# Kernel tuning notes

Hardware: AMD Instinct MI355X
Metric: run time of the kernel (lower is better)

Reference implementation:

```python
import jax, jax.numpy as jnp
import numpy as np

N_CLOSEST = 16
OBJECTNESS_THRESH = 0.75


def _masked_softmax(att, mask):
    # softmax over axis 1 restricted to mask; rows with empty mask -> all zeros
    neg = jnp.where(mask, att, -jnp.inf)
    m = jnp.max(neg, axis=1, keepdims=True)
    m = jnp.where(jnp.isfinite(m), m, 0.0)
    e = jnp.where(mask, jnp.exp(att - m), 0.0)
    d = jnp.sum(e, axis=1, keepdims=True)
    return jnp.where(d > 0, e / jnp.maximum(d, 1e-30), 0.0)


def _forward(aggregated_vote_features, ref_obj_features, objectness_scores,
             ref_center_label, aggregated_vote_xyz, emb_table, init_emb,
             W_enc_att, b_enc_att, W_dec_att, b_dec_att, w_full_att, b_full_att,
             W_ih, b_ih, W_hh, b_hh, W_init_h, b_init_h, W_init_c, b_init_c,
             W_fbeta, b_fbeta, W_fc, b_fc, lang_indices, lang_len):
    B, K, VD = aggregated_vote_features.shape
    T = lang_indices.shape[1]

    # --- objectness + distance (top-k closest) masking ---
    objness = jax.nn.softmax(objectness_scores, axis=-1)[:, :, -1]      # [B,K]
    omask = objness > OBJECTNESS_THRESH
    dist = jnp.linalg.norm(ref_center_label[:, None, :] - aggregated_vote_xyz, axis=2)
    dist = jnp.where(omask, dist, jnp.inf)
    closest = -jax.lax.top_k(-dist, N_CLOSEST)[0]                        # k smallest
    max_d = jnp.max(closest, axis=1, keepdims=True)
    object_mask = omask & (dist <= max_d)                                # [B,K]

    enc = aggregated_vote_features                                       # [B,K,VD]
    init_in = jnp.concatenate([enc.mean(axis=1), ref_obj_features], axis=1)
    h0 = init_in @ W_init_h.T + b_init_h                                 # [B,D]
    c0 = init_in @ W_init_c.T + b_init_c

    # encoder attention projection is constant over timesteps
    att1 = jnp.einsum('bkv,av->bka', enc, W_enc_att) + b_enc_att         # [B,K,A]

    # teacher-forcing inputs: <unk> init embedding then caption embeddings
    E = init_emb.shape[-1]
    emb = jnp.concatenate(
        [jnp.broadcast_to(init_emb, (B, E))[:, None, :], emb_table[lang_indices]],
        axis=1)                                                          # [B,T+1,E]
    emb_steps = jnp.swapaxes(emb[:, :T], 0, 1)                           # [T,B,E]
    t_steps = jnp.arange(T)

    def step(carry, xs):
        h, c = carry
        emb_t, t = xs
        # attention
        att2 = h @ W_dec_att.T + b_dec_att                               # [B,A]
        att = jax.nn.relu(att1 + att2[:, None, :]) @ w_full_att + b_full_att[0]  # [B,K]
        alpha = _masked_softmax(att, object_mask)
        awe = jnp.einsum('bkv,bk->bv', enc, alpha)                       # [B,VD]
        gate = jax.nn.sigmoid(h @ W_fbeta.T + b_fbeta)
        awe = gate * awe
        # LSTMCell (torch gate order i,f,g,o)
        x = jnp.concatenate([emb_t, awe, ref_obj_features], axis=1)      # [B,E+VD+OD]
        gates = x @ W_ih.T + b_ih + h @ W_hh.T + b_hh
        i, f, g, o = jnp.split(gates, 4, axis=1)
        c_new = jax.nn.sigmoid(f) * c + jax.nn.sigmoid(i) * jnp.tanh(g)
        h_new = jax.nn.sigmoid(o) * jnp.tanh(c_new)
        # only samples with length > t are decoded (masked equivalent of batch_size_t)
        active = (t < lang_len)[:, None]
        preds = jnp.where(active, h_new @ W_fc.T + b_fc, 0.0)            # [B,V]
        alpha_o = jnp.where(active, alpha, 0.0)
        h = jnp.where(active, h_new, h)
        c = jnp.where(active, c_new, c)
        return (h, c), (preds, alpha_o)

    _, (preds_seq, alpha_seq) = jax.lax.scan(step, (h0, c0), (emb_steps, t_steps))
    predictions = jnp.transpose(preds_seq, (1, 2, 0))                    # [B,V,T]
    alphas = jnp.transpose(alpha_seq, (1, 0, 2))                         # [B,T,K]
    return predictions, alphas, object_mask


def setup_inputs() -> dict:
    key = jax.random.key(0)
    ks = jax.random.split(key, 20)
    B, K, VD, OD, E, A, D, V, T = 128, 128, 128, 256, 300, 512, 512, 4000, 32
    ENC = VD + OD

    def rn(k, shape, s=1.0):
        return jax.random.normal(k, shape, jnp.float32) * s

    return {
        'aggregated_vote_features': rn(ks[0], (B, K, VD)),
        'ref_obj_features': rn(ks[1], (B, OD)),
        'objectness_scores': rn(ks[2], (B, K, 2)),
        'ref_center_label': rn(ks[3], (B, 3)),
        'aggregated_vote_xyz': rn(ks[4], (B, K, 3)),
        'lang_indices': jax.random.randint(ks[5], (B, T), 0, V),
        'lang_len': jax.random.randint(ks[6], (B,), 1, T + 1),
        'emb_table': rn(ks[7], (V, E), 0.1),
        'init_emb': rn(ks[8], (1, E), 0.1),
        'W_enc_att': rn(ks[9], (A, VD), 0.05), 'b_enc_att': jnp.zeros((A,)),
        'W_dec_att': rn(ks[10], (A, D), 0.05), 'b_dec_att': jnp.zeros((A,)),
        'w_full_att': rn(ks[11], (A,), 0.05), 'b_full_att': jnp.zeros((1,)),
        'W_ih': rn(ks[12], (4 * D, E + ENC), 0.05), 'b_ih': jnp.zeros((4 * D,)),
        'W_hh': rn(ks[13], (4 * D, D), 0.05), 'b_hh': jnp.zeros((4 * D,)),
        'W_init_h': rn(ks[14], (D, ENC), 0.05), 'b_init_h': jnp.zeros((D,)),
        'W_init_c': rn(ks[15], (D, ENC), 0.05), 'b_init_c': jnp.zeros((D,)),
        'W_fbeta': rn(ks[16], (VD, D), 0.05), 'b_fbeta': jnp.zeros((VD,)),
        'W_fc': rn(ks[17], (V, D), 0.1), 'b_fc': jnp.zeros((V,)),
    }


def reference(aggregated_vote_features, ref_obj_features, objectness_scores,
              ref_center_label, aggregated_vote_xyz, lang_indices, lang_len,
              emb_table, init_emb, W_enc_att, b_enc_att, W_dec_att, b_dec_att,
              w_full_att, b_full_att, W_ih, b_ih, W_hh, b_hh, W_init_h, b_init_h,
              W_init_c, b_init_c, W_fbeta, b_fbeta, W_fc, b_fc):
    return _forward(aggregated_vote_features, ref_obj_features, objectness_scores,
                    ref_center_label, aggregated_vote_xyz, emb_table, init_emb,
                    W_enc_att, b_enc_att, W_dec_att, b_dec_att, w_full_att, b_full_att,
                    W_ih, b_ih, W_hh, b_hh, W_init_h, b_init_h, W_init_c, b_init_c,
                    W_fbeta, b_fbeta, W_fc, b_fc, lang_indices, lang_len)
```

## Files before the change

kernel.cpp:

```cpp
#include <hip/hip_runtime.h>
#include <hip/hip_bf16.h>
#include <math.h>

#define XKTOT 1196
#define XKP   1216

static __device__ __forceinline__ float sigmoidf_(float x){ return 1.f/(1.f+expf(-x)); }

__global__ __launch_bounds__(256) void k_transpose(const float* __restrict__ in,
                                                   float* __restrict__ out, int R, int C) {
  __shared__ float tile[32][33];
  int c0 = blockIdx.x * 32, r0 = blockIdx.y * 32;
  int tx = threadIdx.x & 31, ty = threadIdx.x >> 5;
  for (int i = 0; i < 32; i += 8) {
    int r = r0 + ty + i, c = c0 + tx;
    tile[ty + i][tx] = (r < R && c < C) ? in[(size_t)r * C + c] : 0.f;
  }
  __syncthreads();
  for (int i = 0; i < 32; i += 8) {
    int c = c0 + ty + i, r = r0 + tx;
    if (c < C && r < R) out[(size_t)c * R + r] = tile[tx][ty + i];
  }
}

__global__ __launch_bounds__(256) void k_wcat(const float* __restrict__ W_ih,
                                              const float* __restrict__ W_hh,
                                              float* __restrict__ Wcat) {
  int j = blockIdx.x;
  for (int c = threadIdx.x; c < XKP; c += 256) {
    float v;
    if (c < 684)        v = W_ih[(size_t)j * 684 + c];
    else if (c < 1196)  v = W_hh[(size_t)j * 512 + (c - 684)];
    else                v = 0.f;
    Wcat[(size_t)j * XKP + c] = v;
  }
}

__global__ __launch_bounds__(128) void k_mask(const float* __restrict__ objs,
                                              const float* __restrict__ rcl,
                                              const float* __restrict__ avx,
                                              const float* __restrict__ enc,
                                              float* __restrict__ maskf,
                                              float* __restrict__ encmean,
                                              float* __restrict__ out_mask) {
  int b = blockIdx.x, k = threadIdx.x;
  __shared__ float dsh[128];
  __shared__ float maxd;
  float s0 = objs[(size_t)(b * 128 + k) * 2 + 0];
  float s1 = objs[(size_t)(b * 128 + k) * 2 + 1];
  float mx = fmaxf(s0, s1);
  float e0 = expf(s0 - mx), e1 = expf(s1 - mx);
  float p  = e1 / (e0 + e1);
  bool om  = p > 0.75f;
  float dx = rcl[b * 3 + 0] - avx[(size_t)(b * 128 + k) * 3 + 0];
  float dy = rcl[b * 3 + 1] - avx[(size_t)(b * 128 + k) * 3 + 1];
  float dz = rcl[b * 3 + 2] - avx[(size_t)(b * 128 + k) * 3 + 2];
  float dist = sqrtf(dx * dx + dy * dy + dz * dz);
  float dm = om ? dist : INFINITY;
  dsh[k] = dm;
  __syncthreads();
  float v = dm; int clt = 0, cle = 0;
  for (int j = 0; j < 128; j++) { float o = dsh[j]; clt += (o < v); cle += (o <= v); }
  if (clt < 16 && cle >= 16) maxd = v;
  __syncthreads();
  bool msk = om && (dm <= maxd);
  maskf[b * 128 + k]    = msk ? 1.f : 0.f;
  out_mask[b * 128 + k] = msk ? 1.f : 0.f;
  float s = 0.f;
  for (int kk = 0; kk < 128; kk++) s += enc[(size_t)(b * 128 + kk) * 128 + k];
  encmean[b * 128 + k] = s * (1.f / 128.f);
}

__global__ __launch_bounds__(512) void k_init(const float* __restrict__ encm,
                                              const float* __restrict__ rof,
                                              const float* __restrict__ wihT,
                                              const float* __restrict__ wicT,
                                              const float* __restrict__ bh,
                                              const float* __restrict__ bc,
                                              float* __restrict__ h, float* __restrict__ c) {
  int b = blockIdx.x, d = threadIdx.x;
  __shared__ float xin[384];
  if (d < 128) xin[d] = encm[b * 128 + d];
  else if (d < 384) xin[d] = rof[(size_t)b * 256 + (d - 128)];
  __syncthreads();
  float ah = bh[d], ac = bc[d];
  for (int i = 0; i < 384; i++) {
    float x = xin[i];
    ah += x * wihT[(size_t)i * 512 + d];
    ac += x * wicT[(size_t)i * 512 + d];
  }
  h[(size_t)b * 512 + d] = ah;
  c[(size_t)b * 512 + d] = ac;
}

__global__ __launch_bounds__(512) void k_att1(const float* __restrict__ enc,
                                              const float* __restrict__ weT,
                                              const float* __restrict__ b_enc,
                                              float* __restrict__ att1) {
  int b = blockIdx.x >> 3, k0 = (blockIdx.x & 7) * 16;
  int a = threadIdx.x;
  __shared__ float es[16][128];
  for (int i = threadIdx.x; i < 16 * 128; i += 512)
    es[i >> 7][i & 127] = enc[(size_t)(b * 128 + k0 + (i >> 7)) * 128 + (i & 127)];
  __syncthreads();
  float acc[16];
  float bb = b_enc[a];
#pragma unroll
  for (int kk = 0; kk < 16; kk++) acc[kk] = bb;
  for (int i = 0; i < 128; i++) {
    float w = weT[(size_t)i * 512 + a];
#pragma unroll
    for (int kk = 0; kk < 16; kk++) acc[kk] += w * es[kk][i];
  }
#pragma unroll
  for (int kk = 0; kk < 16; kk++)
    att1[(size_t)(b * 128 + k0 + kk) * 512 + a] = acc[kk];
}

__global__ __launch_bounds__(512) void k_step_att(
    const float* __restrict__ att1, const float* __restrict__ h,
    const float* __restrict__ wdT, const float* __restrict__ b_dec,
    const float* __restrict__ wfull, const float* __restrict__ bfull,
    const float* __restrict__ enc, const float* __restrict__ maskf,
    const float* __restrict__ wfbT, const float* __restrict__ b_fbeta,
    const float* __restrict__ rof, const float* __restrict__ embt,
    const float* __restrict__ iemb, const int* __restrict__ lidx,
    const int* __restrict__ llen, float* __restrict__ X,
    float* __restrict__ alphas_out, int t) {
  int b = blockIdx.x, tid = threadIdx.x;
  __shared__ float hs[512], att2[512], wf[512], attk[128], alph[128], awes[128];
  __shared__ float red1[2], red2[2];
  hs[tid] = h[(size_t)b * 512 + tid];
  wf[tid] = wfull[tid];
  __syncthreads();
  {
    float acc = b_dec[tid];
    for (int i = 0; i < 512; i++) acc += hs[i] * wdT[(size_t)i * 512 + tid];
    att2[tid] = acc;
  }
  __syncthreads();
  int k = tid >> 2, j = tid & 3;
  {
    const float4* a1 = (const float4*)(att1 + (size_t)(b * 128 + k) * 512 + j * 128);
    float s = 0.f;
#pragma unroll 4
    for (int i = 0; i < 32; i++) {
      float4 v = a1[i];
      int base = j * 128 + i * 4;
      s += fmaxf(v.x + att2[base + 0], 0.f) * wf[base + 0];
      s += fmaxf(v.y + att2[base + 1], 0.f) * wf[base + 1];
      s += fmaxf(v.z + att2[base + 2], 0.f) * wf[base + 2];
      s += fmaxf(v.w + att2[base + 3], 0.f) * wf[base + 3];
    }
    s += __shfl_xor(s, 1);
    s += __shfl_xor(s, 2);
    if (j == 0) attk[k] = s + bfull[0];
  }
  __syncthreads();
  float mk = 0.f, av = 0.f;
  if (tid < 128) { mk = maskf[b * 128 + tid]; av = attk[tid]; }
  float nv = (tid < 128 && mk != 0.f) ? av : -INFINITY;
  float wm = nv;
#pragma unroll
  for (int o = 32; o > 0; o >>= 1) wm = fmaxf(wm, __shfl_xor(wm, o));
  if (tid < 128 && (tid & 63) == 0) red1[tid >> 6] = wm;
  __syncthreads();
  float m = fmaxf(red1[0], red1[1]);
  float e = 0.f;
  if (tid < 128 && mk != 0.f) e = expf(av - m);
  float sred = e;
#pragma unroll
  for (int o = 32; o > 0; o >>= 1) sred += __shfl_xor(sred, o);
  if (tid < 128 && (tid & 63) == 0) red2[tid >> 6] = sred;
  __syncthreads();
  float dsum = red2[0] + red2[1];
  float alpha = (dsum > 0.f) ? e / fmaxf(dsum, 1e-30f) : 0.f;
  int active = t < llen[b];
  if (tid < 128) {
    alph[tid] = alpha;
    alphas_out[(size_t)(b * 32 + t) * 128 + tid] = active ? alpha : 0.f;
  }
  __syncthreads();
  float awe_v = 0.f;
  if (tid < 128) {
    for (int kk = 0; kk < 128; kk++)
      awe_v += alph[kk] * enc[(size_t)(b * 128 + kk) * 128 + tid];
  }
  {
    int v = tid >> 2;
    float g = 0.f;
    for (int ii = 0; ii < 128; ii++) {
      int i = j * 128 + ii;
      g += hs[i] * wfbT[(size_t)i * 128 + v];
    }
    g += __shfl_xor(g, 1);
    g += __shfl_xor(g, 2);
    if (j == 0) attk[v] = sigmoidf_(g + b_fbeta[v]);
  }
  __syncthreads();
  if (tid < 128) awes[tid] = awe_v * attk[tid];
  __syncthreads();
  const float* esrc = (t == 0) ? iemb : (embt + (size_t)lidx[b * 32 + (t - 1)] * 300);
  for (int c = tid; c < XKP; c += 512) {
    float val;
    if (c < 300)       val = esrc[c];
    else if (c < 428)  val = awes[c - 300];
    else if (c < 684)  val = rof[(size_t)b * 256 + (c - 428)];
    else if (c < 1196) val = hs[c - 684];
    else               val = 0.f;
    X[(size_t)b * XKP + c] = val;
  }
}

__global__ __launch_bounds__(256) void k_gemm(const float* __restrict__ Am, int lda,
                                              const float* __restrict__ Bw, int ldb, int N,
                                              int klen, float* __restrict__ Cpart, int ldc) {
  int n0 = blockIdx.x * 64;
  int m0 = blockIdx.y * 64;
  int kstart = blockIdx.z * klen;
  float* Cout = Cpart + (size_t)blockIdx.z * 128 * ldc;
  int tc = threadIdx.x & 15, tr = threadIdx.x >> 4;
  __shared__ float As[16][68];
  __shared__ float Bs[16][68];
  float acc[4][4];
#pragma unroll
  for (int r = 0; r < 4; r++)
#pragma unroll
    for (int cc = 0; cc < 4; cc++) acc[r][cc] = 0.f;
  int srow = threadIdx.x >> 2, sq = threadIdx.x & 3;
  bool bok = (n0 + srow) < N;
  const float* aSrc = Am + (size_t)(m0 + srow) * lda + sq * 4;
  const float* bSrc = Bw + (size_t)(n0 + srow) * ldb + sq * 4;
  for (int k0 = kstart; k0 < kstart + klen; k0 += 16) {
    float4 va = *(const float4*)(aSrc + k0);
    float4 vb;
    if (bok) vb = *(const float4*)(bSrc + k0);
    else { vb.x = vb.y = vb.z = vb.w = 0.f; }
    As[sq * 4 + 0][srow] = va.x; As[sq * 4 + 1][srow] = va.y;
    As[sq * 4 + 2][srow] = va.z; As[sq * 4 + 3][srow] = va.w;
    Bs[sq * 4 + 0][srow] = vb.x; Bs[sq * 4 + 1][srow] = vb.y;
    Bs[sq * 4 + 2][srow] = vb.z; Bs[sq * 4 + 3][srow] = vb.w;
    __syncthreads();
#pragma unroll
    for (int ki = 0; ki < 16; ki++) {
      float4 a  = *(const float4*)&As[ki][tr * 4];
      float4 bv = *(const float4*)&Bs[ki][tc * 4];
      acc[0][0] += a.x * bv.x; acc[0][1] += a.x * bv.y; acc[0][2] += a.x * bv.z; acc[0][3] += a.x * bv.w;
      acc[1][0] += a.y * bv.x; acc[1][1] += a.y * bv.y; acc[1][2] += a.y * bv.z; acc[1][3] += a.y * bv.w;
      acc[2][0] += a.z * bv.x; acc[2][1] += a.z * bv.y; acc[2][2] += a.z * bv.z; acc[2][3] += a.z * bv.w;
      acc[3][0] += a.w * bv.x; acc[3][1] += a.w * bv.y; acc[3][2] += a.w * bv.z; acc[3][3] += a.w * bv.w;
    }
    __syncthreads();
  }
#pragma unroll
  for (int r = 0; r < 4; r++) {
    int mi = m0 + tr * 4 + r;
#pragma unroll
    for (int cc = 0; cc < 4; cc++) {
      int n = n0 + tc * 4 + cc;
      if (n < N) Cout[(size_t)mi * ldc + n] = acc[r][cc];
    }
  }
}

__global__ __launch_bounds__(256) void k_lstm(const float* __restrict__ gpart,
                                              const float* __restrict__ b_ih,
                                              const float* __restrict__ b_hh,
                                              const int* __restrict__ llen,
                                              float* __restrict__ h, float* __restrict__ c,
                                              int t) {
  int idx = blockIdx.x * 256 + threadIdx.x;
  int b = idx >> 9, d = idx & 511;
  if (t >= llen[b]) return;
  float g4[4];
#pragma unroll
  for (int g = 0; g < 4; g++) {
    int j = g * 512 + d;
    float s = b_ih[j] + b_hh[j];
#pragma unroll
    for (int z = 0; z < 4; z++) s += gpart[((size_t)z * 128 + b) * 2048 + j];
    g4[g] = s;
  }
  float i_ = sigmoidf_(g4[0]);
  float f_ = sigmoidf_(g4[1]);
  float gg = tanhf(g4[2]);
  float o_ = sigmoidf_(g4[3]);
  float cn = f_ * c[idx] + i_ * gg;
  float hn = o_ * tanhf(cn);
  c[idx] = cn;
  h[idx] = hn;
}

__global__ __launch_bounds__(256) void k_fc_red(const float* __restrict__ fpart,
                                                const float* __restrict__ b_fc,
                                                const int* __restrict__ llen,
                                                float* __restrict__ dst, int t, int direct) {
  int idx = blockIdx.x * 256 + threadIdx.x;
  int b = idx / 4000, v = idx - b * 4000;
  float s = 0.f;
  if (t < llen[b])
    s = fpart[(size_t)b * 4000 + v] + fpart[(size_t)(128 + b) * 4000 + v] + b_fc[v];
  if (direct) dst[((size_t)b * 4000 + v) * 32 + t] = s;
  else        dst[((size_t)t * 128 + b) * 4000 + v] = s;
}

__global__ __launch_bounds__(256) void k_out_tr(const float* __restrict__ predsT,
                                                float* __restrict__ out) {
  __shared__ float tile[32][33];
  int b = blockIdx.y, v0 = blockIdx.x * 32;
  int tx = threadIdx.x & 31, ty = threadIdx.x >> 5;
  for (int i = 0; i < 32; i += 8) {
    int tt = ty + i;
    tile[tt][tx] = predsT[((size_t)tt * 128 + b) * 4000 + v0 + tx];
  }
  __syncthreads();
  for (int i = 0; i < 32; i += 8) {
    int v = v0 + ty + i;
    out[((size_t)b * 4000 + v) * 32 + tx] = tile[tx][ty + i];
  }
}

extern "C" void kernel_launch(void* const* d_in, const int* in_sizes, int n_in,
                              void* d_out, int out_size, void* d_ws, size_t ws_size,
                              hipStream_t stream) {
  (void)in_sizes; (void)n_in; (void)out_size;
  const float* avf   = (const float*)d_in[0];
  const float* rof   = (const float*)d_in[1];
  const float* objs  = (const float*)d_in[2];
  const float* rcl   = (const float*)d_in[3];
  const float* avx   = (const float*)d_in[4];
  const int*   lidx  = (const int*)d_in[5];
  const int*   llen  = (const int*)d_in[6];
  const float* embt  = (const float*)d_in[7];
  const float* iemb  = (const float*)d_in[8];
  const float* W_enc = (const float*)d_in[9];
  const float* b_enc = (const float*)d_in[10];
  const float* W_dec = (const float*)d_in[11];
  const float* b_dec = (const float*)d_in[12];
  const float* wfull = (const float*)d_in[13];
  const float* bfull = (const float*)d_in[14];
  const float* W_ih  = (const float*)d_in[15];
  const float* b_ih  = (const float*)d_in[16];
  const float* W_hh  = (const float*)d_in[17];
  const float* b_hh  = (const float*)d_in[18];
  const float* W_inh = (const float*)d_in[19];
  const float* b_inh = (const float*)d_in[20];
  const float* W_inc = (const float*)d_in[21];
  const float* b_inc = (const float*)d_in[22];
  const float* W_fb  = (const float*)d_in[23];
  const float* b_fb  = (const float*)d_in[24];
  const float* W_fc  = (const float*)d_in[25];
  const float* b_fc  = (const float*)d_in[26];

  float* ws = (float*)d_ws;
  size_t f = 0;
  auto A8 = [&](size_t n) { size_t o = f; f += (n + 63) & ~(size_t)63; return o; };
  float* att1  = ws + A8((size_t)128 * 128 * 512);
  float* Wcat  = ws + A8((size_t)2048 * XKP);
  float* wdT   = ws + A8(512 * 512);
  float* weT   = ws + A8(128 * 512);
  float* wihT  = ws + A8(384 * 512);
  float* wicT  = ws + A8(384 * 512);
  float* wfbT  = ws + A8(512 * 128);
  float* hbuf  = ws + A8(128 * 512);
  float* cbuf  = ws + A8(128 * 512);
  float* Xbuf  = ws + A8((size_t)128 * XKP);
  float* maskf = ws + A8(128 * 128);
  float* encm  = ws + A8(128 * 128);
  float* gpart = ws + A8((size_t)4 * 128 * 2048);
  float* fpart = ws + A8((size_t)2 * 128 * 4000);
  float* predsT = ws + A8((size_t)32 * 128 * 4000);
  bool useT = ws_size >= f * sizeof(float);

  float* out_pred  = (float*)d_out;
  float* out_alpha = out_pred + (size_t)16384000;
  float* out_mask  = out_alpha + (size_t)524288;

  k_transpose<<<dim3(16, 16), 256, 0, stream>>>(W_dec, wdT, 512, 512);
  k_transpose<<<dim3(4, 16),  256, 0, stream>>>(W_enc, weT, 512, 128);
  k_transpose<<<dim3(12, 16), 256, 0, stream>>>(W_inh, wihT, 512, 384);
  k_transpose<<<dim3(12, 16), 256, 0, stream>>>(W_inc, wicT, 512, 384);
  k_transpose<<<dim3(16, 4),  256, 0, stream>>>(W_fb, wfbT, 128, 512);
  k_wcat<<<2048, 256, 0, stream>>>(W_ih, W_hh, Wcat);
  k_mask<<<128, 128, 0, stream>>>(objs, rcl, avx, avf, maskf, encm, out_mask);
  k_init<<<128, 512, 0, stream>>>(encm, rof, wihT, wicT, b_inh, b_inc, hbuf, cbuf);
  k_att1<<<1024, 512, 0, stream>>>(avf, weT, b_enc, att1);

  for (int t = 0; t < 32; t++) {
    k_step_att<<<128, 512, 0, stream>>>(att1, hbuf, wdT, b_dec, wfull, bfull,
        avf, maskf, wfbT, b_fb, rof, embt, iemb, lidx, llen, Xbuf, out_alpha, t);
    k_gemm<<<dim3(32, 2, 4), 256, 0, stream>>>(Xbuf, XKP, Wcat, XKP, 2048, 304, gpart, 2048);
    k_lstm<<<256, 256, 0, stream>>>(gpart, b_ih, b_hh, llen, hbuf, cbuf, t);
    k_gemm<<<dim3(63, 2, 2), 256, 0, stream>>>(hbuf, 512, W_fc, 512, 4000, 256, fpart, 4000);
    k_fc_red<<<2000, 256, 0, stream>>>(fpart, b_fc, llen,
                                       useT ? predsT : out_pred, t, useT ? 0 : 1);
  }
  if (useT) k_out_tr<<<dim3(125, 128), 256, 0, stream>>>(predsT, out_pred);
}
```

Baseline: 2.730 ms.

## Move LSTM gate, FC and attention projections onto bf16 MFMA with split precision

Replaces the fp32 SIMT GEMMs with bf16 MFMA kernels. The LSTM gate GEMM uses hi/lo split bf16 (three products) to keep near-fp32 accuracy and fuses the LSTM cell update into its epilogue. The FC projection is also fused with bias, masking and store, which removes the split-K partial buffers and the separate reduction kernels. The encoder attention projection and FC now run in plain bf16, which adds conversion kernels and some rounding error.

```diff
diff --git a/kernel.cpp b/kernel.cpp
--- a/kernel.cpp
+++ b/kernel.cpp
@@ -5,7 +5,13 @@
 #define XKTOT 1196
 #define XKP   1216
 
+typedef unsigned short u16;
+typedef short bf16x8 __attribute__((ext_vector_type(8)));
+typedef float f32x4 __attribute__((ext_vector_type(4)));
+
 static __device__ __forceinline__ float sigmoidf_(float x){ return 1.f/(1.f+expf(-x)); }
+static __device__ __forceinline__ u16 f2bf(float x){ __hip_bfloat16 h = __float2bfloat16(x); return *reinterpret_cast<u16*>(&h); }
+static __device__ __forceinline__ float bf2f(u16 u){ __hip_bfloat16 h; *reinterpret_cast<u16*>(&h) = u; return __bfloat162float(h); }
 
 __global__ __launch_bounds__(256) void k_transpose(const float* __restrict__ in,
                                                    float* __restrict__ out, int R, int C) {
@@ -23,16 +29,28 @@
   }
 }
 
-__global__ __launch_bounds__(256) void k_wcat(const float* __restrict__ W_ih,
-                                              const float* __restrict__ W_hh,
-                                              float* __restrict__ Wcat) {
-  int j = blockIdx.x;
+__global__ __launch_bounds__(256) void k_cvt(const float* __restrict__ in,
+                                             u16* __restrict__ out, int n) {
+  for (int i = blockIdx.x * 256 + threadIdx.x; i < n; i += gridDim.x * 256)
+    out[i] = f2bf(in[i]);
+}
+
+__global__ __launch_bounds__(256) void k_wcat_split(const float* __restrict__ W_ih,
+                                                    const float* __restrict__ W_hh,
+                                                    u16* __restrict__ Whi,
+                                                    u16* __restrict__ Wlo) {
+  int np = blockIdx.x;
+  int d = np >> 2, g = np & 3;
+  int j = g * 512 + d;
   for (int c = threadIdx.x; c < XKP; c += 256) {
     float v;
     if (c < 684)        v = W_ih[(size_t)j * 684 + c];
     else if (c < 1196)  v = W_hh[(size_t)j * 512 + (c - 684)];
     else                v = 0.f;
-    Wcat[(size_t)j * XKP + c] = v;
+    u16 hi = f2bf(v);
+    u16 lo = f2bf(v - bf2f(hi));
+    Whi[(size_t)np * XKP + c] = hi;
+    Wlo[(size_t)np * XKP + c] = lo;
   }
 }
 
@@ -77,7 +95,8 @@
                                               const float* __restrict__ wicT,
                                               const float* __restrict__ bh,
                                               const float* __restrict__ bc,
-                                              float* __restrict__ h, float* __restrict__ c) {
+                                              float* __restrict__ h, float* __restrict__ c,
+                                              u16* __restrict__ hb16) {
   int b = blockIdx.x, d = threadIdx.x;
   __shared__ float xin[384];
   if (d < 128) xin[d] = encm[b * 128 + d];
@@ -89,32 +108,45 @@
     ah += x * wihT[(size_t)i * 512 + d];
     ac += x * wicT[(size_t)i * 512 + d];
   }
-  h[(size_t)b * 512 + d] = ah;
-  c[(size_t)b * 512 + d] = ac;
-}
-
-__global__ __launch_bounds__(512) void k_att1(const float* __restrict__ enc,
-                                              const float* __restrict__ weT,
-                                              const float* __restrict__ b_enc,
-                                              float* __restrict__ att1) {
-  int b = blockIdx.x >> 3, k0 = (blockIdx.x & 7) * 16;
-  int a = threadIdx.x;
-  __shared__ float es[16][128];
-  for (int i = threadIdx.x; i < 16 * 128; i += 512)
-    es[i >> 7][i & 127] = enc[(size_t)(b * 128 + k0 + (i >> 7)) * 128 + (i & 127)];
-  __syncthreads();
-  float acc[16];
-  float bb = b_enc[a];
-#pragma unroll
-  for (int kk = 0; kk < 16; kk++) acc[kk] = bb;
-  for (int i = 0; i < 128; i++) {
-    float w = weT[(size_t)i * 512 + a];
-#pragma unroll
-    for (int kk = 0; kk < 16; kk++) acc[kk] += w * es[kk][i];
-  }
-#pragma unroll
-  for (int kk = 0; kk < 16; kk++)
-    att1[(size_t)(b * 128 + k0 + kk) * 512 + a] = acc[kk];
+  size_t idx = (size_t)b * 512 + d;
+  h[idx] = ah;
+  c[idx] = ac;
+  hb16[idx] = f2bf(ah);
+}
+
+__global__ __launch_bounds__(256) void k_att1m(const u16* __restrict__ enc16,
+                                               const u16* __restrict__ We16,
+                                               const float* __restrict__ b_enc,
+                                               float* __restrict__ att1) {
+  int w = threadIdx.x >> 6, lane = threadIdx.x & 63;
+  int gw = blockIdx.x * 4 + w;
+  int nt = gw & 15, mt = gw >> 4;
+  int m0 = mt * 32, n0 = nt * 32;
+  int rc = lane & 15, kb = lane >> 4;
+  const bf16x8* a0 = (const bf16x8*)(enc16 + (size_t)(m0 + rc) * 128) + kb;
+  const bf16x8* a1 = (const bf16x8*)(enc16 + (size_t)(m0 + 16 + rc) * 128) + kb;
+  const bf16x8* b0 = (const bf16x8*)(We16 + (size_t)(n0 + rc) * 128) + kb;
+  const bf16x8* b1 = (const bf16x8*)(We16 + (size_t)(n0 + 16 + rc) * 128) + kb;
+  f32x4 z = {0.f, 0.f, 0.f, 0.f};
+  f32x4 acc00 = z, acc01 = z, acc10 = z, acc11 = z;
+#pragma unroll
+  for (int kk = 0; kk < 4; kk++) {
+    bf16x8 av0 = a0[kk * 4], av1 = a1[kk * 4];
+    bf16x8 bv0 = b0[kk * 4], bv1 = b1[kk * 4];
+    acc00 = __builtin_amdgcn_mfma_f32_16x16x32_bf16(av0, bv0, acc00, 0, 0, 0);
+    acc01 = __builtin_amdgcn_mfma_f32_16x16x32_bf16(av0, bv1, acc01, 0, 0, 0);
+    acc10 = __builtin_amdgcn_mfma_f32_16x16x32_bf16(av1, bv0, acc10, 0, 0, 0);
+    acc11 = __builtin_amdgcn_mfma_f32_16x16x32_bf16(av1, bv1, acc11, 0, 0, 0);
+  }
+  int col = lane & 15, rbase = (lane >> 4) * 4;
+#pragma unroll
+  for (int r = 0; r < 4; r++) {
+    int r0g = m0 + rbase + r;
+    att1[(size_t)r0g * 512 + n0 + col]        = acc00[r] + b_enc[n0 + col];
+    att1[(size_t)r0g * 512 + n0 + 16 + col]   = acc01[r] + b_enc[n0 + 16 + col];
+    att1[(size_t)(r0g + 16) * 512 + n0 + col]      = acc10[r] + b_enc[n0 + col];
+    att1[(size_t)(r0g + 16) * 512 + n0 + 16 + col] = acc11[r] + b_enc[n0 + 16 + col];
+  }
 }
 
 __global__ __launch_bounds__(512) void k_step_att(
@@ -125,7 +157,7 @@
     const float* __restrict__ wfbT, const float* __restrict__ b_fbeta,
     const float* __restrict__ rof, const float* __restrict__ embt,
     const float* __restrict__ iemb, const int* __restrict__ lidx,
-    const int* __restrict__ llen, float* __restrict__ X,
+    const int* __restrict__ llen, u16* __restrict__ Xhi, u16* __restrict__ Xlo,
     float* __restrict__ alphas_out, int t) {
   int b = blockIdx.x, tid = threadIdx.x;
   __shared__ float hs[512], att2[512], wf[512], attk[128], alph[128], awes[128];
@@ -208,100 +240,91 @@
     else if (c < 684)  val = rof[(size_t)b * 256 + (c - 428)];
     else if (c < 1196) val = hs[c - 684];
     else               val = 0.f;
-    X[(size_t)b * XKP + c] = val;
-  }
-}
-
-__global__ __launch_bounds__(256) void k_gemm(const float* __restrict__ Am, int lda,
-                                              const float* __restrict__ Bw, int ldb, int N,
-                                              int klen, float* __restrict__ Cpart, int ldc) {
-  int n0 = blockIdx.x * 64;
-  int m0 = blockIdx.y * 64;
-  int kstart = blockIdx.z * klen;
-  float* Cout = Cpart + (size_t)blockIdx.z * 128 * ldc;
-  int tc = threadIdx.x & 15, tr = threadIdx.x >> 4;
-  __shared__ float As[16][68];
-  __shared__ float Bs[16][68];
-  float acc[4][4];
-#pragma unroll
-  for (int r = 0; r < 4; r++)
-#pragma unroll
-    for (int cc = 0; cc < 4; cc++) acc[r][cc] = 0.f;
-  int srow = threadIdx.x >> 2, sq = threadIdx.x & 3;
-  bool bok = (n0 + srow) < N;
-  const float* aSrc = Am + (size_t)(m0 + srow) * lda + sq * 4;
-  const float* bSrc = Bw + (size_t)(n0 + srow) * ldb + sq * 4;
-  for (int k0 = kstart; k0 < kstart + klen; k0 += 16) {
-    float4 va = *(const float4*)(aSrc + k0);
-    float4 vb;
-    if (bok) vb = *(const float4*)(bSrc + k0);
-    else { vb.x = vb.y = vb.z = vb.w = 0.f; }
-    As[sq * 4 + 0][srow] = va.x; As[sq * 4 + 1][srow] = va.y;
-    As[sq * 4 + 2][srow] = va.z; As[sq * 4 + 3][srow] = va.w;
-    Bs[sq * 4 + 0][srow] = vb.x; Bs[sq * 4 + 1][srow] = vb.y;
-    Bs[sq * 4 + 2][srow] = vb.z; Bs[sq * 4 + 3][srow] = vb.w;
-    __syncthreads();
-#pragma unroll
-    for (int ki = 0; ki < 16; ki++) {
-      float4 a  = *(const float4*)&As[ki][tr * 4];
-      float4 bv = *(const float4*)&Bs[ki][tc * 4];
-      acc[0][0] += a.x * bv.x; acc[0][1] += a.x * bv.y; acc[0][2] += a.x * bv.z; acc[0][3] += a.x * bv.w;
-      acc[1][0] += a.y * bv.x; acc[1][1] += a.y * bv.y; acc[1][2] += a.y * bv.z; acc[1][3] += a.y * bv.w;
-      acc[2][0] += a.z * bv.x; acc[2][1] += a.z * bv.y; acc[2][2] += a.z * bv.z; acc[2][3] += a.z * bv.w;
-      acc[3][0] += a.w * bv.x; acc[3][1] += a.w * bv.y; acc[3][2] += a.w * bv.z; acc[3][3] += a.w * bv.w;
+    u16 hi = f2bf(val);
+    Xhi[(size_t)b * XKP + c] = hi;
+    Xlo[(size_t)b * XKP + c] = f2bf(val - bf2f(hi));
+  }
+}
+
+__global__ __launch_bounds__(256) void k_gates(const u16* __restrict__ Xhi,
+                                               const u16* __restrict__ Xlo,
+                                               const u16* __restrict__ Whi,
+                                               const u16* __restrict__ Wlo,
+                                               const float* __restrict__ b_ih,
+                                               const float* __restrict__ b_hh,
+                                               const int* __restrict__ llen,
+                                               float* __restrict__ h, float* __restrict__ c,
+                                               u16* __restrict__ hb16, int t) {
+  int w = threadIdx.x >> 6, lane = threadIdx.x & 63;
+  int mt = blockIdx.x >> 5;
+  int nt = (blockIdx.x & 31) * 4 + w;
+  int m0 = mt * 16, n0 = nt * 16;
+  int rc = lane & 15, kb = lane >> 4;
+  const bf16x8* aHi = (const bf16x8*)(Xhi + (size_t)(m0 + rc) * XKP) + kb;
+  const bf16x8* aLo = (const bf16x8*)(Xlo + (size_t)(m0 + rc) * XKP) + kb;
+  const bf16x8* bHi = (const bf16x8*)(Whi + (size_t)(n0 + rc) * XKP) + kb;
+  const bf16x8* bLo = (const bf16x8*)(Wlo + (size_t)(n0 + rc) * XKP) + kb;
+  f32x4 acc = {0.f, 0.f, 0.f, 0.f};
+#pragma unroll 2
+  for (int kk = 0; kk < 38; kk++) {
+    bf16x8 ah = aHi[kk * 4], al = aLo[kk * 4];
+    bf16x8 bh = bHi[kk * 4], bl = bLo[kk * 4];
+    acc = __builtin_amdgcn_mfma_f32_16x16x32_bf16(ah, bh, acc, 0, 0, 0);
+    acc = __builtin_amdgcn_mfma_f32_16x16x32_bf16(al, bh, acc, 0, 0, 0);
+    acc = __builtin_amdgcn_mfma_f32_16x16x32_bf16(ah, bl, acc, 0, 0, 0);
+  }
+  __shared__ float tile[4][16][17];
+#pragma unroll
+  for (int r = 0; r < 4; r++) tile[w][(lane >> 4) * 4 + r][lane & 15] = acc[r];
+  __syncthreads();
+  int lb = lane & 15, ld = lane >> 4;
+  int b = m0 + lb, d = nt * 4 + ld;
+  if (t < llen[b]) {
+    float g4[4];
+#pragma unroll
+    for (int g = 0; g < 4; g++) {
+      int jj = g * 512 + d;
+      g4[g] = tile[w][lb][ld * 4 + g] + b_ih[jj] + b_hh[jj];
     }
-    __syncthreads();
-  }
+    float i_ = sigmoidf_(g4[0]);
+    float f_ = sigmoidf_(g4[1]);
+    float gg = tanhf(g4[2]);
+    float o_ = sigmoidf_(g4[3]);
+    size_t idx = (size_t)b * 512 + d;
+    float cn = f_ * c[idx] + i_ * gg;
+    float hn = o_ * tanhf(cn);
+    c[idx] = cn;
+    h[idx] = hn;
+    hb16[idx] = f2bf(hn);
+  }
+}
+
+__global__ __launch_bounds__(256) void k_fc(const u16* __restrict__ hb16,
+                                            const u16* __restrict__ Wfc16,
+                                            const float* __restrict__ b_fc,
+                                            const int* __restrict__ llen,
+                                            float* __restrict__ dst, int t, int direct) {
+  int w = threadIdx.x >> 6, lane = threadIdx.x & 63;
+  int gw = blockIdx.x * 4 + w;
+  int mt = gw & 7, nt = gw >> 3;
+  int m0 = mt * 16, n0 = nt * 16;
+  int rc = lane & 15, kb = lane >> 4;
+  const bf16x8* aP = (const bf16x8*)(hb16 + (size_t)(m0 + rc) * 512) + kb;
+  const bf16x8* bP = (const bf16x8*)(Wfc16 + (size_t)(n0 + rc) * 512) + kb;
+  f32x4 acc = {0.f, 0.f, 0.f, 0.f};
+#pragma unroll 4
+  for (int kk = 0; kk < 16; kk++)
+    acc = __builtin_amdgcn_mfma_f32_16x16x32_bf16(aP[kk * 4], bP[kk * 4], acc, 0, 0, 0);
+  int col = lane & 15, rbase = (lane >> 4) * 4;
+  int v = n0 + col;
+  float bias = b_fc[v];
 #pragma unroll
   for (int r = 0; r < 4; r++) {
-    int mi = m0 + tr * 4 + r;
-#pragma unroll
-    for (int cc = 0; cc < 4; cc++) {
-      int n = n0 + tc * 4 + cc;
-      if (n < N) Cout[(size_t)mi * ldc + n] = acc[r][cc];
-    }
-  }
-}
-
-__global__ __launch_bounds__(256) void k_lstm(const float* __restrict__ gpart,
-                                              const float* __restrict__ b_ih,
-                                              const float* __restrict__ b_hh,
-                                              const int* __restrict__ llen,
-                                              float* __restrict__ h, float* __restrict__ c,
-                                              int t) {
-  int idx = blockIdx.x * 256 + threadIdx.x;
-  int b = idx >> 9, d = idx & 511;
-  if (t >= llen[b]) return;
-  float g4[4];
-#pragma unroll
-  for (int g = 0; g < 4; g++) {
-    int j = g * 512 + d;
-    float s = b_ih[j] + b_hh[j];
-#pragma unroll
-    for (int z = 0; z < 4; z++) s += gpart[((size_t)z * 128 + b) * 2048 + j];
-    g4[g] = s;
-  }
-  float i_ = sigmoidf_(g4[0]);
-  float f_ = sigmoidf_(g4[1]);
-  float gg = tanhf(g4[2]);
-  float o_ = sigmoidf_(g4[3]);
-  float cn = f_ * c[idx] + i_ * gg;
-  float hn = o_ * tanhf(cn);
-  c[idx] = cn;
-  h[idx] = hn;
-}
-
-__global__ __launch_bounds__(256) void k_fc_red(const float* __restrict__ fpart,
-                                                const float* __restrict__ b_fc,
-                                                const int* __restrict__ llen,
-                                                float* __restrict__ dst, int t, int direct) {
-  int idx = blockIdx.x * 256 + threadIdx.x;
-  int b = idx / 4000, v = idx - b * 4000;
-  float s = 0.f;
-  if (t < llen[b])
-    s = fpart[(size_t)b * 4000 + v] + fpart[(size_t)(128 + b) * 4000 + v] + b_fc[v];
-  if (direct) dst[((size_t)b * 4000 + v) * 32 + t] = s;
-  else        dst[((size_t)t * 128 + b) * 4000 + v] = s;
+    int b = m0 + rbase + r;
+    float val = (t < llen[b]) ? (acc[r] + bias) : 0.f;
+    if (direct) dst[((size_t)b * 4000 + v) * 32 + t] = val;
+    else        dst[((size_t)(t * 128 + b)) * 4000 + v] = val;
+  }
 }
 
 __global__ __launch_bounds__(256) void k_out_tr(const float* __restrict__ predsT,
@@ -356,20 +379,23 @@
   size_t f = 0;
   auto A8 = [&](size_t n) { size_t o = f; f += (n + 63) & ~(size_t)63; return o; };
   float* att1  = ws + A8((size_t)128 * 128 * 512);
-  float* Wcat  = ws + A8((size_t)2048 * XKP);
   float* wdT   = ws + A8(512 * 512);
-  float* weT   = ws + A8(128 * 512);
   float* wihT  = ws + A8(384 * 512);
   float* wicT  = ws + A8(384 * 512);
   float* wfbT  = ws + A8(512 * 128);
   float* hbuf  = ws + A8(128 * 512);
   float* cbuf  = ws + A8(128 * 512);
-  float* Xbuf  = ws + A8((size_t)128 * XKP);
   float* maskf = ws + A8(128 * 128);
   float* encm  = ws + A8(128 * 128);
-  float* gpart = ws + A8((size_t)4 * 128 * 2048);
-  float* fpart = ws + A8((size_t)2 * 128 * 4000);
-  float* predsT = ws + A8((size_t)32 * 128 * 4000);
+  u16*   Xhi   = (u16*)(ws + A8((size_t)128 * XKP / 2));
+  u16*   Xlo   = (u16*)(ws + A8((size_t)128 * XKP / 2));
+  u16*   WcatHi= (u16*)(ws + A8((size_t)2048 * XKP / 2));
+  u16*   WcatLo= (u16*)(ws + A8((size_t)2048 * XKP / 2));
+  u16*   enc16 = (u16*)(ws + A8((size_t)128 * 128 * 128 / 2));
+  u16*   We16  = (u16*)(ws + A8((size_t)512 * 128 / 2));
+  u16*   Wfc16 = (u16*)(ws + A8((size_t)4000 * 512 / 2));
+  u16*   hb16  = (u16*)(ws + A8((size_t)128 * 512 / 2));
+  float* predsT= ws + A8((size_t)32 * 128 * 4000);
   bool useT = ws_size >= f * sizeof(float);
 
   float* out_pred  = (float*)d_out;
@@ -377,23 +403,24 @@
   float* out_mask  = out_alpha + (size_t)524288;
 
   k_transpose<<<dim3(16, 16), 256, 0, stream>>>(W_dec, wdT, 512, 512);
-  k_transpose<<<dim3(4, 16),  256, 0, stream>>>(W_enc, weT, 512, 128);
   k_transpose<<<dim3(12, 16), 256, 0, stream>>>(W_inh, wihT, 512, 384);
   k_transpose<<<dim3(12, 16), 256, 0, stream>>>(W_inc, wicT, 512, 384);
   k_transpose<<<dim3(16, 4),  256, 0, stream>>>(W_fb, wfbT, 128, 512);
-  k_wcat<<<2048, 256, 0, stream>>>(W_ih, W_hh, Wcat);
+  k_wcat_split<<<2048, 256, 0, stream>>>(W_ih, W_hh, WcatHi, WcatLo);
+  k_cvt<<<2048, 256, 0, stream>>>(avf, enc16, 128 * 128 * 128);
+  k_cvt<<<256,  256, 0, stream>>>(W_enc, We16, 512 * 128);
+  k_cvt<<<2048, 256, 0, stream>>>(W_fc, Wfc16, 4000 * 512);
   k_mask<<<128, 128, 0, stream>>>(objs, rcl, avx, avf, maskf, encm, out_mask);
-  k_init<<<128, 512, 0, stream>>>(encm, rof, wihT, wicT, b_inh, b_inc, hbuf, cbuf);
-  k_att1<<<1024, 512, 0, stream>>>(avf, weT, b_enc, att1);
+  k_init<<<128, 512, 0, stream>>>(encm, rof, wihT, wicT, b_inh, b_inc, hbuf, cbuf, hb16);
+  k_att1m<<<2048, 256, 0, stream>>>(enc16, We16, b_enc, att1);
 
   for (int t = 0; t < 32; t++) {
     k_step_att<<<128, 512, 0, stream>>>(att1, hbuf, wdT, b_dec, wfull, bfull,
-        avf, maskf, wfbT, b_fb, rof, embt, iemb, lidx, llen, Xbuf, out_alpha, t);
-    k_gemm<<<dim3(32, 2, 4), 256, 0, stream>>>(Xbuf, XKP, Wcat, XKP, 2048, 304, gpart, 2048);
-    k_lstm<<<256, 256, 0, stream>>>(gpart, b_ih, b_hh, llen, hbuf, cbuf, t);
-    k_gemm<<<dim3(63, 2, 2), 256, 0, stream>>>(hbuf, 512, W_fc, 512, 4000, 256, fpart, 4000);
-    k_fc_red<<<2000, 256, 0, stream>>>(fpart, b_fc, llen,
-                                       useT ? predsT : out_pred, t, useT ? 0 : 1);
+        avf, maskf, wfbT, b_fb, rof, embt, iemb, lidx, llen, Xhi, Xlo, out_alpha, t);
+    k_gates<<<256, 256, 0, stream>>>(Xhi, Xlo, WcatHi, WcatLo, b_ih, b_hh, llen,
+                                     hbuf, cbuf, hb16, t);
+    k_fc<<<500, 256, 0, stream>>>(hb16, Wfc16, b_fc, llen,
+                                  useT ? predsT : out_pred, t, useT ? 0 : 1);
   }
   if (useT) k_out_tr<<<dim3(125, 128), 256, 0, stream>>>(predsT, out_pred);
 }
```

After: 2.435 ms. 10.8% less time.
